# Kernel optimization log

Measured on AMD Instinct MI355X. Metric: run time of the kernel, lower is better.

## Reference

```python
import jax, jax.numpy as jnp
import numpy as np

N, E, FIN, NH, FOUT = 50000, 800000, 128, 4, 16


def setup_inputs() -> dict:
    key = jax.random.key(0)
    ks = jax.random.split(key, 6)
    x = jax.random.normal(ks[0], (N, FIN), dtype=jnp.float32)
    edge_index = jax.random.randint(ks[1], (2, E), 0, N, dtype=jnp.int64)
    w_proj = jax.random.normal(ks[2], (NH * FOUT, FIN), dtype=jnp.float32) * 0.05
    a_src = jax.random.normal(ks[3], (NH, FOUT), dtype=jnp.float32) * 0.1
    a_trg = jax.random.normal(ks[4], (NH, FOUT), dtype=jnp.float32) * 0.1
    w_skip = jax.random.normal(ks[5], (NH * FOUT, FIN), dtype=jnp.float32) * 0.05
    return {"x": x, "edge_index": edge_index, "w_proj": w_proj,
            "a_src": a_src, "a_trg": a_trg, "w_skip": w_skip}


def reference(x, edge_index, w_proj, a_src, a_trg, w_skip):
    # Dropout is identity in eval mode.
    src, trg = edge_index[0], edge_index[1]
    # Project: [N, NH, FOUT]
    proj = (x @ w_proj.T).reshape(N, NH, FOUT)
    # Per-node attention logits: [N, NH]
    s_src = jnp.einsum('nhf,hf->nh', proj, a_src)
    s_trg = jnp.einsum('nhf,hf->nh', proj, a_trg)
    # Lift to edges and score: [E, NH]
    scores = jax.nn.leaky_relu(s_src[src] + s_trg[trg], negative_slope=0.2)
    # Global-max-shifted exp (matches original, which subtracts the global max)
    exp_scores = jnp.exp(scores - jnp.max(scores))
    # Segment-wise softmax denominator over target nodes
    denom = jax.ops.segment_sum(exp_scores, trg, num_segments=N)  # [N, NH]
    attn = exp_scores / (denom[trg] + 1e-16)                      # [E, NH]
    # Weighted aggregation of lifted source features: [N, NH, FOUT]
    weighted = proj[src] * attn[:, :, None]
    agg = jax.ops.segment_sum(weighted, trg, num_segments=N)
    # Skip projection (FOUT != FIN branch) and concat over heads
    out = agg + (x @ w_skip.T).reshape(N, NH, FOUT)
    out = out.reshape(N, NH * FOUT)
    return jax.nn.elu(out)
```

## Files before the change

### kernel.cpp

```cpp
#include <hip/hip_runtime.h>
#include <cstddef>

#define N_NODES 50000
#define N_EDGES 800000
#define FIN     128
#define NH      4
#define FOUT    16
#define COUT    64
#define STRIPS  (N_NODES / 16)
#define SCAN_BLOCKS ((N_NODES + 255) / 256)
#define NB      128
#define CHUNK   (N_EDGES / NB)
#define HW4     (N_NODES / 4)
#define HBYTES  (HW4 * 4)

typedef __bf16 bf16x8 __attribute__((ext_vector_type(8)));
typedef float  f32x4  __attribute__((ext_vector_type(4)));

__global__ __launch_bounds__(256) void k0_init(
    const float* __restrict__ wproj, const float* __restrict__ wskip,
    __bf16* __restrict__ wb)
{
    int gid = blockIdx.x * 256 + threadIdx.x;
    if (gid < (128 * FIN) / 4) {
        int row = gid >> 5;
        float4 v = (row < 64) ? reinterpret_cast<const float4*>(wproj)[gid]
                              : reinterpret_cast<const float4*>(wskip)[gid - 2048];
        __bf16* o = wb + (size_t)gid * 4;
        o[0] = (__bf16)v.x; o[1] = (__bf16)v.y;
        o[2] = (__bf16)v.z; o[3] = (__bf16)v.w;
    }
}

__global__ __launch_bounds__(256) void k1_mfma(
    const float* __restrict__ x, const __bf16* __restrict__ wb,
    const float* __restrict__ asrc, const float* __restrict__ atrg,
    __bf16* __restrict__ projb, float* __restrict__ ssrc, float* __restrict__ strg,
    float* __restrict__ outv)
{
    const int lane  = threadIdx.x & 63;
    const int wid   = blockIdx.x * 4 + (threadIdx.x >> 6);
    const int strip = wid >> 1;
    const int half  = wid & 1;
    if (strip >= STRIPS) return;
    const int r = lane & 15;
    const int g = lane >> 4;
    const int row0 = strip * 16;

    bf16x8 bfr[4][4];
    #pragma unroll
    for (int j = 0; j < 4; ++j) {
        const __bf16* wrow = wb + (size_t)(half * 64 + j * 16 + r) * FIN;
        #pragma unroll
        for (int kk = 0; kk < 4; ++kk)
            bfr[j][kk] = *reinterpret_cast<const bf16x8*>(wrow + kk * 32 + g * 8);
    }

    const float* xrow = x + (size_t)(row0 + r) * FIN + g * 8;
    bf16x8 afr[4];
    #pragma unroll
    for (int kk = 0; kk < 4; ++kk) {
        float4 u0 = *reinterpret_cast<const float4*>(xrow + kk * 32);
        float4 u1 = *reinterpret_cast<const float4*>(xrow + kk * 32 + 4);
        bf16x8 a;
        a[0] = (__bf16)u0.x; a[1] = (__bf16)u0.y;
        a[2] = (__bf16)u0.z; a[3] = (__bf16)u0.w;
        a[4] = (__bf16)u1.x; a[5] = (__bf16)u1.y;
        a[6] = (__bf16)u1.z; a[7] = (__bf16)u1.w;
        afr[kk] = a;
    }

    f32x4 acc[4] = {{0.f,0.f,0.f,0.f},{0.f,0.f,0.f,0.f},
                    {0.f,0.f,0.f,0.f},{0.f,0.f,0.f,0.f}};
    #pragma unroll
    for (int kk = 0; kk < 4; ++kk)
        #pragma unroll
        for (int j = 0; j < 4; ++j)
            acc[j] = __builtin_amdgcn_mfma_f32_16x16x32_bf16(
                         afr[kk], bfr[j][kk], acc[j], 0, 0, 0);

    if (!half) {
        #pragma unroll
        for (int j = 0; j < 4; ++j)
            #pragma unroll
            for (int q = 0; q < 4; ++q)
                projb[(size_t)(row0 + g * 4 + q) * COUT + j * 16 + r] =
                    (__bf16)acc[j][q];
        #pragma unroll
        for (int j = 0; j < 4; ++j) {
            const float as = asrc[j * 16 + r];
            const float at = atrg[j * 16 + r];
            #pragma unroll
            for (int q = 0; q < 4; ++q) {
                float ts = acc[j][q] * as;
                float tt = acc[j][q] * at;
                ts += __shfl_xor(ts, 1); ts += __shfl_xor(ts, 2);
                ts += __shfl_xor(ts, 4); ts += __shfl_xor(ts, 8);
                tt += __shfl_xor(tt, 1); tt += __shfl_xor(tt, 2);
                tt += __shfl_xor(tt, 4); tt += __shfl_xor(tt, 8);
                if (r == 0) {
                    int n = row0 + g * 4 + q;
                    ssrc[(size_t)n * NH + j] = ts;
                    strg[(size_t)n * NH + j] = tt;
                }
            }
        }
    } else {
        #pragma unroll
        for (int j = 0; j < 4; ++j)
            #pragma unroll
            for (int q = 0; q < 4; ++q)
                outv[(size_t)(row0 + g * 4 + q) * COUT + j * 16 + r] = acc[j][q];
    }
}

__global__ __launch_bounds__(1024) void k_hist(
    const int* __restrict__ ei, unsigned* __restrict__ histG)
{
    extern __shared__ unsigned h[];
    const int t = threadIdx.x;
    for (int i = t; i < HW4; i += 1024) h[i] = 0;
    __syncthreads();
    const int base = blockIdx.x * CHUNK;
    for (int i = t; i < CHUNK; i += 1024) {
        int tg = ei[N_EDGES + base + i];
        atomicAdd(&h[tg >> 2], 1u << ((tg & 3) * 8));
    }
    __syncthreads();
    unsigned* out = histG + (size_t)blockIdx.x * HW4;
    for (int i = t; i < HW4; i += 1024) out[i] = h[i];
}

__global__ __launch_bounds__(256) void k_colscan(
    const unsigned* __restrict__ histG, unsigned* __restrict__ offG,
    int* __restrict__ deg)
{
    int p = blockIdx.x * 256 + threadIdx.x;
    if (p >= HW4) return;
    unsigned run = 0;
    for (int b = 0; b < NB; ++b) {
        unsigned v = histG[(size_t)b * HW4 + p];
        offG[(size_t)b * HW4 + p] = run;
        run += v;
    }
    reinterpret_cast<int4*>(deg)[p] =
        make_int4((int)(run & 0xffu), (int)((run >> 8) & 0xffu),
                  (int)((run >> 16) & 0xffu), (int)(run >> 24));
}

__global__ __launch_bounds__(256) void scan_a(
    const int* __restrict__ deg, int* __restrict__ tmpExc, int* __restrict__ bsum)
{
    __shared__ int sm[256];
    int t = threadIdx.x;
    int i = blockIdx.x * 256 + t;
    int v = (i < N_NODES) ? deg[i] : 0;
    sm[t] = v; __syncthreads();
    #pragma unroll
    for (int off = 1; off < 256; off <<= 1) {
        int x = (t >= off) ? sm[t - off] : 0;
        __syncthreads();
        sm[t] += x;
        __syncthreads();
    }
    if (i < N_NODES) tmpExc[i] = sm[t] - v;
    if (t == 255) bsum[blockIdx.x] = sm[t];
}

__global__ __launch_bounds__(256) void scan_b(
    const int* __restrict__ bsum, int* __restrict__ bOff)
{
    __shared__ int sm[256];
    int t = threadIdx.x;
    int v = (t < SCAN_BLOCKS) ? bsum[t] : 0;
    sm[t] = v; __syncthreads();
    #pragma unroll
    for (int off = 1; off < 256; off <<= 1) {
        int x = (t >= off) ? sm[t - off] : 0;
        __syncthreads();
        sm[t] += x;
        __syncthreads();
    }
    if (t < SCAN_BLOCKS) bOff[t] = sm[t] - v;
}

__global__ __launch_bounds__(1024) void k_place(
    const int* __restrict__ ei, const unsigned* __restrict__ offG,
    const int* __restrict__ tmpExc, const int* __restrict__ bOff,
    int* __restrict__ srcs)
{
    extern __shared__ unsigned h[];
    const int t = threadIdx.x;
    for (int i = t; i < HW4; i += 1024) h[i] = 0;
    __syncthreads();
    const int base = blockIdx.x * CHUNK;
    const unsigned* off = offG + (size_t)blockIdx.x * HW4;
    for (int i = t; i < CHUNK; i += 1024) {
        int s  = ei[base + i];
        int tg = ei[N_EDGES + base + i];
        int sh = (tg & 3) * 8;
        unsigned old = atomicAdd(&h[tg >> 2], 1u << sh);
        int local = (int)((old >> sh) & 0xffu);
        int cross = (int)((off[tg >> 2] >> sh) & 0xffu);
        int slot  = tmpExc[tg] + bOff[tg >> 8] + cross + local;
        srcs[slot] = s;
    }
}

__global__ __launch_bounds__(256) void k3_gather(
    const int* __restrict__ tmpExc, const int* __restrict__ bOff,
    const int* __restrict__ deg, const int* __restrict__ srcs,
    const float* __restrict__ ssrc, const float* __restrict__ strg,
    const __bf16* __restrict__ projb, float* __restrict__ outv)
{
    const int lane = threadIdx.x & 63;
    const int node = __builtin_amdgcn_readfirstlane(blockIdx.x * 4 + (threadIdx.x >> 6));
    if (node >= N_NODES) return;
    const int h = lane >> 4;
    const int begin = tmpExc[node] + bOff[node >> 8];
    const int dg    = deg[node];
    const float st  = strg[(size_t)node * NH + h];
    const float skip = outv[(size_t)node * COUT + lane];

    float acc = 0.f, dsum = 0.f;
    int i = 0;
    for (; i + 8 <= dg; i += 8) {
        int s[8]; float a[8], p[8];
        #pragma unroll
        for (int u = 0; u < 8; ++u) s[u] = srcs[begin + i + u];
        #pragma unroll
        for (int u = 0; u < 8; ++u) a[u] = ssrc[(size_t)s[u] * NH + h];
        #pragma unroll
        for (int u = 0; u < 8; ++u) p[u] = (float)projb[(size_t)s[u] * COUT + lane];
        #pragma unroll
        for (int u = 0; u < 8; ++u) {
            float z = a[u] + st;
            z = (z >= 0.f) ? z : 0.2f * z;
            float ez = __expf(z);
            dsum += ez;
            acc += ez * p[u];
        }
    }
    for (; i + 4 <= dg; i += 4) {
        int s[4]; float a[4], p[4];
        #pragma unroll
        for (int u = 0; u < 4; ++u) s[u] = srcs[begin + i + u];
        #pragma unroll
        for (int u = 0; u < 4; ++u) a[u] = ssrc[(size_t)s[u] * NH + h];
        #pragma unroll
        for (int u = 0; u < 4; ++u) p[u] = (float)projb[(size_t)s[u] * COUT + lane];
        #pragma unroll
        for (int u = 0; u < 4; ++u) {
            float z = a[u] + st;
            z = (z >= 0.f) ? z : 0.2f * z;
            float ez = __expf(z);
            dsum += ez;
            acc += ez * p[u];
        }
    }
    for (; i < dg; ++i) {
        int s = srcs[begin + i];
        float z = ssrc[(size_t)s * NH + h] + st;
        z = (z >= 0.f) ? z : 0.2f * z;
        float ez = __expf(z);
        float p  = (float)projb[(size_t)s * COUT + lane];
        dsum += ez;
        acc += ez * p;
    }
    float o = acc / (dsum + 1e-16f) + skip;
    o = (o > 0.f) ? o : expm1f(o);
    outv[(size_t)node * COUT + lane] = o;
}

extern "C" void kernel_launch(void* const* d_in, const int* in_sizes, int n_in,
                              void* d_out, int out_size, void* d_ws, size_t ws_size,
                              hipStream_t stream)
{
    const float* x     = (const float*)d_in[0];
    const int*   ei    = (const int*)  d_in[1];
    const float* wproj = (const float*)d_in[2];
    const float* asrc  = (const float*)d_in[3];
    const float* atrg  = (const float*)d_in[4];
    const float* wskip = (const float*)d_in[5];
    float* outv = (float*)d_out;

    __bf16* projb = (__bf16*)d_ws;
    float* base  = (float*)d_ws;
    float* ssrc  = base + (size_t)N_NODES * COUT;
    float* strg  = ssrc + (size_t)N_NODES * NH;
    int* deg     = (int*)(strg + (size_t)N_NODES * NH);
    int* tmpExc  = deg    + N_NODES;
    int* bsum    = tmpExc + N_NODES;
    int* bOff    = bsum   + 256;
    int* srcs    = bOff   + 256;
    unsigned* histG = (unsigned*)(srcs + N_EDGES);
    unsigned* offG  = histG + (size_t)NB * HW4;
    __bf16* wb   = (__bf16*)(offG + (size_t)NB * HW4);

    k0_init<<<16, 256, 0, stream>>>(wproj, wskip, wb);

    int k1_blocks = (STRIPS * 2 + 3) / 4;
    k1_mfma<<<k1_blocks, 256, 0, stream>>>(x, wb, asrc, atrg,
                                           projb, ssrc, strg, outv);

    k_hist<<<NB, 1024, HBYTES, stream>>>(ei, histG);

    k_colscan<<<(HW4 + 255) / 256, 256, 0, stream>>>(histG, offG, deg);

    scan_a<<<SCAN_BLOCKS, 256, 0, stream>>>(deg, tmpExc, bsum);
    scan_b<<<1, 256, 0, stream>>>(bsum, bOff);

    k_place<<<NB, 1024, HBYTES, stream>>>(ei, offG, tmpExc, bOff, srcs);

    int k3_blocks = (N_NODES + 3) / 4;
    k3_gather<<<k3_blocks, 256, 0, stream>>>(tmpExc, bOff, deg, srcs,
                                             ssrc, strg, projb, outv);
}
```

Measured before the change: 105.5 us.

## Split column scan into four parallel segments and fuse weight conversion into MFMA kernel

The serial column scan over 128 histogram blocks becomes a two-level scan: four segments are scanned in parallel through a 2D grid, then a small kernel adds the segment bases, which k_place now folds into its cross offset. The goal is to cut the long dependent loop in the colscan kernel, which previously ran on only about 49 blocks. Separately, the weight-to-bf16 conversion kernel is removed and each MFMA wave converts fp32 weights itself. This drops one launch but adds redundant weight loads and conversions in every wave, plus an extra kernel and an extra buffer read in k_place.

```diff
diff --git a/kernel.cpp b/kernel.cpp
--- a/kernel.cpp
+++ b/kernel.cpp
@@ -13,27 +13,16 @@
 #define CHUNK   (N_EDGES / NB)
 #define HW4     (N_NODES / 4)
 #define HBYTES  (HW4 * 4)
+#define NQ      4
+#define BPQ     (NB / NQ)
+#define PBLK    ((HW4 + 255) / 256)
 
 typedef __bf16 bf16x8 __attribute__((ext_vector_type(8)));
 typedef float  f32x4  __attribute__((ext_vector_type(4)));
 
-__global__ __launch_bounds__(256) void k0_init(
+__global__ __launch_bounds__(256) void k1_mfma(
+    const float* __restrict__ x,
     const float* __restrict__ wproj, const float* __restrict__ wskip,
-    __bf16* __restrict__ wb)
-{
-    int gid = blockIdx.x * 256 + threadIdx.x;
-    if (gid < (128 * FIN) / 4) {
-        int row = gid >> 5;
-        float4 v = (row < 64) ? reinterpret_cast<const float4*>(wproj)[gid]
-                              : reinterpret_cast<const float4*>(wskip)[gid - 2048];
-        __bf16* o = wb + (size_t)gid * 4;
-        o[0] = (__bf16)v.x; o[1] = (__bf16)v.y;
-        o[2] = (__bf16)v.z; o[3] = (__bf16)v.w;
-    }
-}
-
-__global__ __launch_bounds__(256) void k1_mfma(
-    const float* __restrict__ x, const __bf16* __restrict__ wb,
     const float* __restrict__ asrc, const float* __restrict__ atrg,
     __bf16* __restrict__ projb, float* __restrict__ ssrc, float* __restrict__ strg,
     float* __restrict__ outv)
@@ -46,14 +35,23 @@
     const int r = lane & 15;
     const int g = lane >> 4;
     const int row0 = strip * 16;
+    const float* __restrict__ W = half ? wskip : wproj;
 
     bf16x8 bfr[4][4];
     #pragma unroll
     for (int j = 0; j < 4; ++j) {
-        const __bf16* wrow = wb + (size_t)(half * 64 + j * 16 + r) * FIN;
-        #pragma unroll
-        for (int kk = 0; kk < 4; ++kk)
-            bfr[j][kk] = *reinterpret_cast<const bf16x8*>(wrow + kk * 32 + g * 8);
+        const float* wrow = W + (size_t)(j * 16 + r) * FIN + g * 8;
+        #pragma unroll
+        for (int kk = 0; kk < 4; ++kk) {
+            float4 u0 = *reinterpret_cast<const float4*>(wrow + kk * 32);
+            float4 u1 = *reinterpret_cast<const float4*>(wrow + kk * 32 + 4);
+            bf16x8 b;
+            b[0] = (__bf16)u0.x; b[1] = (__bf16)u0.y;
+            b[2] = (__bf16)u0.z; b[3] = (__bf16)u0.w;
+            b[4] = (__bf16)u1.x; b[5] = (__bf16)u1.y;
+            b[6] = (__bf16)u1.z; b[7] = (__bf16)u1.w;
+            bfr[j][kk] = b;
+        }
     }
 
     const float* xrow = x + (size_t)(row0 + r) * FIN + g * 8;
@@ -131,21 +129,38 @@
     for (int i = t; i < HW4; i += 1024) out[i] = h[i];
 }
 
-__global__ __launch_bounds__(256) void k_colscan(
+__global__ __launch_bounds__(256) void k_colscanA(
     const unsigned* __restrict__ histG, unsigned* __restrict__ offG,
-    int* __restrict__ deg)
+    unsigned* __restrict__ partial)
 {
     int p = blockIdx.x * 256 + threadIdx.x;
     if (p >= HW4) return;
+    int q = blockIdx.y;
     unsigned run = 0;
-    for (int b = 0; b < NB; ++b) {
+    #pragma unroll 4
+    for (int b = q * BPQ; b < (q + 1) * BPQ; ++b) {
         unsigned v = histG[(size_t)b * HW4 + p];
         offG[(size_t)b * HW4 + p] = run;
         run += v;
     }
+    partial[(size_t)q * HW4 + p] = run;
+}
+
+__global__ __launch_bounds__(256) void k_colscanB(
+    const unsigned* __restrict__ partial, unsigned* __restrict__ baseQ,
+    int* __restrict__ deg)
+{
+    int p = blockIdx.x * 256 + threadIdx.x;
+    if (p >= HW4) return;
+    unsigned s = 0;
+    #pragma unroll
+    for (int q = 0; q < NQ; ++q) {
+        baseQ[(size_t)q * HW4 + p] = s;
+        s += partial[(size_t)q * HW4 + p];
+    }
     reinterpret_cast<int4*>(deg)[p] =
-        make_int4((int)(run & 0xffu), (int)((run >> 8) & 0xffu),
-                  (int)((run >> 16) & 0xffu), (int)(run >> 24));
+        make_int4((int)(s & 0xffu), (int)((s >> 8) & 0xffu),
+                  (int)((s >> 16) & 0xffu), (int)(s >> 24));
 }
 
 __global__ __launch_bounds__(256) void scan_a(
@@ -186,6 +201,7 @@
 
 __global__ __launch_bounds__(1024) void k_place(
     const int* __restrict__ ei, const unsigned* __restrict__ offG,
+    const unsigned* __restrict__ baseQ,
     const int* __restrict__ tmpExc, const int* __restrict__ bOff,
     int* __restrict__ srcs)
 {
@@ -194,14 +210,16 @@
     for (int i = t; i < HW4; i += 1024) h[i] = 0;
     __syncthreads();
     const int base = blockIdx.x * CHUNK;
-    const unsigned* off = offG + (size_t)blockIdx.x * HW4;
+    const unsigned* off = offG  + (size_t)blockIdx.x * HW4;
+    const unsigned* bq  = baseQ + (size_t)(blockIdx.x / BPQ) * HW4;
     for (int i = t; i < CHUNK; i += 1024) {
         int s  = ei[base + i];
         int tg = ei[N_EDGES + base + i];
         int sh = (tg & 3) * 8;
         unsigned old = atomicAdd(&h[tg >> 2], 1u << sh);
         int local = (int)((old >> sh) & 0xffu);
-        int cross = (int)((off[tg >> 2] >> sh) & 0xffu);
+        unsigned cw = off[tg >> 2] + bq[tg >> 2];
+        int cross = (int)((cw >> sh) & 0xffu);
         int slot  = tmpExc[tg] + bOff[tg >> 8] + cross + local;
         srcs[slot] = s;
     }
@@ -293,24 +311,24 @@
     int* bsum    = tmpExc + N_NODES;
     int* bOff    = bsum   + 256;
     int* srcs    = bOff   + 256;
-    unsigned* histG = (unsigned*)(srcs + N_EDGES);
-    unsigned* offG  = histG + (size_t)NB * HW4;
-    __bf16* wb   = (__bf16*)(offG + (size_t)NB * HW4);
-
-    k0_init<<<16, 256, 0, stream>>>(wproj, wskip, wb);
+    unsigned* histG   = (unsigned*)(srcs + N_EDGES);
+    unsigned* offG    = histG + (size_t)NB * HW4;
+    unsigned* partial = offG  + (size_t)NB * HW4;
+    unsigned* baseQ   = partial + (size_t)NQ * HW4;
 
     int k1_blocks = (STRIPS * 2 + 3) / 4;
-    k1_mfma<<<k1_blocks, 256, 0, stream>>>(x, wb, asrc, atrg,
+    k1_mfma<<<k1_blocks, 256, 0, stream>>>(x, wproj, wskip, asrc, atrg,
                                            projb, ssrc, strg, outv);
 
     k_hist<<<NB, 1024, HBYTES, stream>>>(ei, histG);
 
-    k_colscan<<<(HW4 + 255) / 256, 256, 0, stream>>>(histG, offG, deg);
+    k_colscanA<<<dim3(PBLK, NQ), 256, 0, stream>>>(histG, offG, partial);
+    k_colscanB<<<PBLK, 256, 0, stream>>>(partial, baseQ, deg);
 
     scan_a<<<SCAN_BLOCKS, 256, 0, stream>>>(deg, tmpExc, bsum);
     scan_b<<<1, 256, 0, stream>>>(bsum, bOff);
 
-    k_place<<<NB, 1024, HBYTES, stream>>>(ei, offG, tmpExc, bOff, srcs);
+    k_place<<<NB, 1024, HBYTES, stream>>>(ei, offG, baseQ, tmpExc, bOff, srcs);
 
     int k3_blocks = (N_NODES + 3) / 4;
     k3_gather<<<k3_blocks, 256, 0, stream>>>(tmpExc, bOff, deg, srcs,
```

Measured after the change: 115.6 us. 1.1x slower.
